# Performance work log

Hardware: AMD Instinct MI355X
Metric: run time of the kernel (lower is better)

Reference implementation:

```python
import jax, jax.numpy as jnp
import numpy as np

B, C, H, W = 4, 256, 64, 64
CQK = C // 8


def setup_inputs() -> dict:
    key = jax.random.key(0)
    ks = jax.random.split(key, 7)
    s = 1.0 / np.sqrt(C)
    return {
        "x": jax.random.normal(ks[0], (B, C, H, W), dtype=jnp.float32),
        "Wq": jax.random.normal(ks[1], (CQK, C), dtype=jnp.float32) * s,
        "bq": jax.random.normal(ks[2], (CQK,), dtype=jnp.float32) * 0.01,
        "Wk": jax.random.normal(ks[3], (CQK, C), dtype=jnp.float32) * s,
        "bk": jax.random.normal(ks[4], (CQK,), dtype=jnp.float32) * 0.01,
        "Wv": jax.random.normal(ks[5], (C, C), dtype=jnp.float32) * s,
        "bv": jax.random.normal(ks[6], (C,), dtype=jnp.float32) * 0.01,
    }


def reference(x, Wq, bq, Wk, bk, Wv, bv):
    b, c, h, w = x.shape
    n = h * w
    xf = x.reshape(b, c, n)                                   # [B,C,N]
    # 1x1 convs == per-pixel channel projections
    q = jnp.einsum('oc,bcn->bon', Wq, xf) + bq[None, :, None]  # [B,C/8,N]
    k = jnp.einsum('oc,bcn->bon', Wk, xf) + bk[None, :, None]  # [B,C/8,N]
    v = jnp.einsum('oc,bcn->bon', Wv, xf) + bv[None, :, None]  # [B,C,N]
    # energy[b,i,j] = <q[:, i], k[:, j]>  (no scaling, as in the original)
    energy = jnp.einsum('boi,boj->bij', q, k)                  # [B,N,N]
    attn = jax.nn.softmax(energy, axis=-1)                     # [B,N,N]
    # out[b,c,i] = sum_j v[b,c,j] * attn[b,i,j]
    out = jnp.einsum('bcj,bij->bci', v, attn)                  # [B,C,N]
    return out.reshape(b, c, h, w) + x
```

## Files before the change

### kernel.cpp

```cpp
#include <hip/hip_runtime.h>
#include <hip/hip_bf16.h>
#include <math.h>

#define B_DIM 4
#define C_DIM 256
#define CQK_DIM 32
#define N_POS 4096
#define NPART 4

typedef unsigned short u16;
typedef __attribute__((ext_vector_type(8))) short bf16x8;
typedef __attribute__((ext_vector_type(4))) float f32x4;

__device__ __forceinline__ u16 f32_to_bf16_rn(float f) {
    union { float f; unsigned int u; } v; v.f = f;
    unsigned int u = v.u;
    u += 0x7fffu + ((u >> 16) & 1u);
    return (u16)(u >> 16);
}
__device__ __forceinline__ float bf16_to_f32(u16 h) {
    union { unsigned int u; float f; } v; v.u = ((unsigned int)h) << 16;
    return v.f;
}
__device__ __forceinline__ unsigned pk_bf16(float a, float b) {
    unsigned r;
    asm("v_cvt_pk_bf16_f32 %0, %1, %2" : "=v"(r) : "v"(a), "v"(b));
    return r;
}
__device__ __forceinline__ void async_copy16(const u16* g, u16* l) {
    __builtin_amdgcn_global_load_lds(
        (const __attribute__((address_space(1))) void*)g,
        (__attribute__((address_space(3))) void*)l, 16, 0, 0);
}


__global__ __launch_bounds__(256) void proj_kernel(
    const float* __restrict__ x,
    const float* __restrict__ Wq, const float* __restrict__ bq,
    const float* __restrict__ Wk, const float* __restrict__ bk,
    const float* __restrict__ Wv, const float* __restrict__ bv,
    u16* __restrict__ qhi, u16* __restrict__ qlo,
    u16* __restrict__ kth, u16* __restrict__ ktl,
    u16* __restrict__ vtile)
{
    const int t    = threadIdx.x;
    const int blk  = blockIdx.x;
    const int b    = blk >> 6;
    const int jt   = blk & 63;
    const int n0   = jt * 64;
    const int wave = t >> 6;
    const int lane = t & 63;
    const int n16  = lane & 15;
    const int quad = lane >> 4;
    const float* xb = x + (size_t)b * C_DIM * N_POS;

    f32x4 accV[4][4];
    f32x4 accQ[4];
    #pragma unroll
    for (int v = 0; v < 4; ++v)
        #pragma unroll
        for (int nt = 0; nt < 4; ++nt) accV[v][nt] = (f32x4){0.f,0.f,0.f,0.f};
    #pragma unroll
    for (int nt = 0; nt < 4; ++nt) accQ[nt] = (f32x4){0.f,0.f,0.f,0.f};

    const float* Wqk  = (wave < 2) ? Wq : Wk;
    const int    qkrow = (wave & 1) * 16 + n16;

    for (int kk = 0; kk < 8; ++kk) {
        const int k0 = kk * 32 + quad * 8;
        bf16x8 bh[4], bl[4];
        #pragma unroll
        for (int nt = 0; nt < 4; ++nt) {
            const float* xp = xb + (size_t)k0 * N_POS + n0 + nt * 16 + n16;
            float xv[8];
            #pragma unroll
            for (int j = 0; j < 8; ++j) xv[j] = xp[(size_t)j * N_POS];
            #pragma unroll
            for (int j = 0; j < 8; ++j) {
                u16 h = f32_to_bf16_rn(xv[j]);
                bh[nt][j] = (short)h;
                bl[nt][j] = (short)f32_to_bf16_rn(xv[j] - bf16_to_f32(h));
            }
        }
        #pragma unroll
        for (int v = 0; v < 4; ++v) {
            const float* wr = Wv + (size_t)(wave * 64 + v * 16 + n16) * C_DIM + k0;
            float4 a0 = *(const float4*)(wr);
            float4 a1 = *(const float4*)(wr + 4);
            bf16x8 ah;
            ah[0] = (short)f32_to_bf16_rn(a0.x); ah[1] = (short)f32_to_bf16_rn(a0.y);
            ah[2] = (short)f32_to_bf16_rn(a0.z); ah[3] = (short)f32_to_bf16_rn(a0.w);
            ah[4] = (short)f32_to_bf16_rn(a1.x); ah[5] = (short)f32_to_bf16_rn(a1.y);
            ah[6] = (short)f32_to_bf16_rn(a1.z); ah[7] = (short)f32_to_bf16_rn(a1.w);
            #pragma unroll
            for (int nt = 0; nt < 4; ++nt)
                accV[v][nt] = __builtin_amdgcn_mfma_f32_16x16x32_bf16(
                    ah, bh[nt], accV[v][nt], 0, 0, 0);
        }
        {
            const float* wr = Wqk + (size_t)qkrow * C_DIM + k0;
            bf16x8 ah, al;
            #pragma unroll
            for (int j = 0; j < 8; ++j) {
                float w = wr[j];
                u16 h = f32_to_bf16_rn(w);
                ah[j] = (short)h;
                al[j] = (short)f32_to_bf16_rn(w - bf16_to_f32(h));
            }
            #pragma unroll
            for (int nt = 0; nt < 4; ++nt) {
                accQ[nt] = __builtin_amdgcn_mfma_f32_16x16x32_bf16(ah, bh[nt], accQ[nt], 0, 0, 0);
                accQ[nt] = __builtin_amdgcn_mfma_f32_16x16x32_bf16(ah, bl[nt], accQ[nt], 0, 0, 0);
                accQ[nt] = __builtin_amdgcn_mfma_f32_16x16x32_bf16(al, bh[nt], accQ[nt], 0, 0, 0);
            }
        }
    }

    u16* vt = vtile + (size_t)(b * 64 + jt) * (32 * 512);
    #pragma unroll
    for (int v = 0; v < 4; ++v) {
        const int cb = wave * 4 + v;
        #pragma unroll
        for (int r = 0; r < 4; ++r) {
            const int c = cb * 16 + quad * 4 + r;
            const float bias = bv[c];
            #pragma unroll
            for (int nt = 0; nt < 4; ++nt) {
                const int kb = nt >> 1;
                vt[(cb * 2 + kb) * 512
                   + ((n16 >> 2) * 16 + quad * 4 + r) * 8
                   + (nt & 1) * 4 + (n16 & 3)] =
                    f32_to_bf16_rn(accV[v][nt][r] + bias);
            }
        }
    }
    if (wave < 2) {
        #pragma unroll
        for (int r = 0; r < 4; ++r) {
            const int c = (wave & 1) * 16 + quad * 4 + r;
            const float bias = bq[c];
            #pragma unroll
            for (int nt = 0; nt < 4; ++nt) {
                float val = accQ[nt][r] + bias;
                u16 h = f32_to_bf16_rn(val);
                u16 lo = f32_to_bf16_rn(val - bf16_to_f32(h));
                size_t base = ((size_t)b * N_POS + n0 + nt * 16 + n16) * CQK_DIM + c;
                qhi[base] = h; qlo[base] = lo;
            }
        }
    } else {
        u16* kh_t = kth + (size_t)(b * 64 + jt) * (4 * 512);
        u16* kl_t = ktl + (size_t)(b * 64 + jt) * (4 * 512);
        #pragma unroll
        for (int r = 0; r < 4; ++r) {
            const int c = (wave & 1) * 16 + quad * 4 + r;
            const float bias = bk[c];
            #pragma unroll
            for (int nt = 0; nt < 4; ++nt) {
                float val = accQ[nt][r] + bias;
                u16 h = f32_to_bf16_rn(val);
                u16 lo = f32_to_bf16_rn(val - bf16_to_f32(h));
                const int off = nt * 512 + ((c >> 3) * 16 + n16) * 8 + (c & 7);
                kh_t[off] = h; kl_t[off] = lo;
            }
        }
    }
}

__global__ __launch_bounds__(256, 2) void flash_kernel(
    const u16* __restrict__ qhi, const u16* __restrict__ qlo,
    const u16* __restrict__ kth, const u16* __restrict__ ktl,
    const u16* __restrict__ vtile,
    u16* __restrict__ part, float2* __restrict__ ml)
{
    __shared__ u16 Vt[2][40 * 512];

    const int t    = threadIdx.x;
    const int wave = t >> 6;
    const int lane = t & 63;
    const int n16  = lane & 15;
    const int quad = lane >> 4;

    const int idx    = blockIdx.x;
    const int xcd    = idx & 7;
    const int b      = xcd & 3;
    const int z      = idx >> 3;
    const int p      = z & 3;
    const int iouter = z >> 2;
    const int itile  = (iouter << 1) | (xcd >> 2);
    const int i0     = itile * 128 + wave * 32;

    bf16x8 qh[2], ql[2];
    #pragma unroll
    for (int m = 0; m < 2; ++m) {
        qh[m] = *(const bf16x8*)(qhi + ((size_t)b * N_POS + i0 + m * 16 + n16) * CQK_DIM + quad * 8);
        ql[m] = *(const bf16x8*)(qlo + ((size_t)b * N_POS + i0 + m * 16 + n16) * CQK_DIM + quad * 8);
    }

    f32x4 O[2][16];
    #pragma unroll
    for (int m = 0; m < 2; ++m)
        #pragma unroll
        for (int cb = 0; cb < 16; ++cb) O[m][cb] = (f32x4){0.f, 0.f, 0.f, 0.f};
    float lsum[2] = {0.f, 0.f};

    const int jt_beg = p * 16;
    const int jt_end = jt_beg + 16;

    const u16* vb_base = vtile + (size_t)b * 64 * (32 * 512);
    const u16* kh_base = kth   + (size_t)b * 64 * (4 * 512);
    const u16* kl_base = ktl   + (size_t)b * 64 * (4 * 512);

#define STAGE(JT, BUF)                                                          \
    {                                                                           \
        const u16* vsrc  = vb_base + (size_t)(JT) * (32 * 512);                 \
        const u16* khsrc = kh_base + (size_t)(JT) * (4 * 512);                  \
        const u16* klsrc = kl_base + (size_t)(JT) * (4 * 512);                  \
        for (int ch = wave; ch < 32; ch += 4)                                   \
            async_copy16(vsrc + ch * 512 + lane * 8, Vt[BUF] + ch * 512);       \
        for (int ch = wave; ch < 8; ch += 4)                                    \
            async_copy16((ch < 4 ? khsrc + ch * 512 : klsrc + (ch - 4) * 512)   \
                             + lane * 8,                                        \
                         Vt[BUF] + (32 + ch) * 512);                            \
    }

    STAGE(jt_beg, 0);

    int buf = 0;
    for (int jt = jt_beg; jt < jt_end; ++jt) {
        __syncthreads();

        if (jt + 1 < jt_end) STAGE(jt + 1, buf ^ 1);

        const u16* kbuf = Vt[buf];
        bf16x8 kh[4], kl[4];
        #pragma unroll
        for (int jb = 0; jb < 4; ++jb) {
            kh[jb] = *(const bf16x8*)(kbuf + (32 + jb) * 512 + lane * 8);
            kl[jb] = *(const bf16x8*)(kbuf + (36 + jb) * 512 + lane * 8);
        }

        f32x4 s[2][4];
        __builtin_amdgcn_s_setprio(1);
        #pragma unroll
        for (int m = 0; m < 2; ++m)
            #pragma unroll
            for (int jb = 0; jb < 4; ++jb) {
                f32x4 acc = (f32x4){0.f, 0.f, 0.f, 0.f};
                acc = __builtin_amdgcn_mfma_f32_16x16x32_bf16(kh[jb], qh[m], acc, 0, 0, 0);
                acc = __builtin_amdgcn_mfma_f32_16x16x32_bf16(kl[jb], qh[m], acc, 0, 0, 0);
                acc = __builtin_amdgcn_mfma_f32_16x16x32_bf16(kh[jb], ql[m], acc, 0, 0, 0);
                s[m][jb] = acc;
            }
        __builtin_amdgcn_s_setprio(0);

        bf16x8 Pf[2][2];
        #pragma unroll
        for (int m = 0; m < 2; ++m)
            #pragma unroll
            for (int kb = 0; kb < 2; ++kb) {
                union { bf16x8 v; unsigned u[4]; } tmp;
                #pragma unroll
                for (int j2 = 0; j2 < 2; ++j2) {
                    const int jb = kb * 2 + j2;
                    float p0 = __expf(s[m][jb][0]);
                    float p1 = __expf(s[m][jb][1]);
                    float p2 = __expf(s[m][jb][2]);
                    float p3 = __expf(s[m][jb][3]);
                    lsum[m] += (p0 + p1) + (p2 + p3);
                    tmp.u[j2 * 2 + 0] = pk_bf16(p0, p1);
                    tmp.u[j2 * 2 + 1] = pk_bf16(p2, p3);
                }
                Pf[m][kb] = tmp.v;
            }

        const u16* vb = Vt[buf];
        __builtin_amdgcn_s_setprio(1);
        #pragma unroll
        for (int kb = 0; kb < 2; ++kb) {
            #pragma unroll
            for (int cb = 0; cb < 16; ++cb) {
                bf16x8 Vf = *(const bf16x8*)(vb + (cb * 2 + kb) * 512 + lane * 8);
                #pragma unroll
                for (int m = 0; m < 2; ++m)
                    O[m][cb] = __builtin_amdgcn_mfma_f32_16x16x32_bf16(
                        Pf[m][kb], Vf, O[m][cb], 0, 0, 0);
            }
        }
        __builtin_amdgcn_s_setprio(0);
        buf ^= 1;
    }
#undef STAGE

    #pragma unroll
    for (int m = 0; m < 2; ++m) {
        lsum[m] += __shfl_xor(lsum[m], 16, 64);
        lsum[m] += __shfl_xor(lsum[m], 32, 64);
    }
    float inv_l[2][4];
    #pragma unroll
    for (int m = 0; m < 2; ++m)
        #pragma unroll
        for (int r = 0; r < 4; ++r)
            inv_l[m][r] = 1.f / __shfl(lsum[m], quad * 4 + r, 64);

    u16* pbase = part + ((size_t)(p * 4 + b) * N_POS + i0) * C_DIM;
    #pragma unroll
    for (int m = 0; m < 2; ++m)
        #pragma unroll
        for (int cb = 0; cb < 16; ++cb)
            #pragma unroll
            for (int r = 0; r < 4; ++r)
                pbase[(size_t)(m * 16 + quad * 4 + r) * C_DIM + cb * 16 + n16] =
                    f32_to_bf16_rn(O[m][cb][r] * inv_l[m][r]);
    if (quad == 0) {
        #pragma unroll
        for (int m = 0; m < 2; ++m)
            ml[(size_t)(p * 4 + b) * N_POS + i0 + m * 16 + n16] =
                make_float2(0.f, lsum[m]);
    }
}

__global__ __launch_bounds__(256) void reduce_kernel(
    const u16* __restrict__ part, const float2* __restrict__ ml,
    const float* __restrict__ x, float* __restrict__ out)
{
    const int TJ = 32;
    __shared__ float wgt[NPART][TJ];
    __shared__ float trans[C_DIM][TJ + 1];

    const int t   = threadIdx.x;
    const int blk = blockIdx.x;
    const int b   = blk >> 7;
    const int n0  = (blk & 127) * TJ;

    if (t < TJ) {
        int i = n0 + t;
        float s = 0.f, w[NPART];
        #pragma unroll
        for (int p = 0; p < NPART; ++p) {
            float2 a = ml[(size_t)(p * 4 + b) * N_POS + i];
            w[p] = a.y;
            s += w[p];
        }
        float inv = 1.f / s;
        #pragma unroll
        for (int p = 0; p < NPART; ++p) wgt[p][t] = w[p] * inv;
    }
    __syncthreads();

    {
        const int cp = t & 127;
        const int ih = t >> 7;
        for (int ib = 0; ib < TJ; ib += 2) {
            int i = ib + ih;
            float acc0 = 0.f, acc1 = 0.f;
            #pragma unroll
            for (int p = 0; p < NPART; ++p) {
                const u16* row = part + ((size_t)(p * 4 + b) * N_POS + n0 + i) * C_DIM;
                ushort2 pv = ((const ushort2*)row)[cp];
                float wp = wgt[p][i];
                acc0 += wp * bf16_to_f32(pv.x);
                acc1 += wp * bf16_to_f32(pv.y);
            }
            trans[2 * cp][i]     = acc0;
            trans[2 * cp + 1][i] = acc1;
        }
    }
    __syncthreads();

    {
        const int il = t & 31;
        const int cr = t >> 5;
        const float* xb = x + (size_t)b * C_DIM * N_POS;
        float* ob       = out + (size_t)b * C_DIM * N_POS;
        for (int cc = 0; cc < 32; ++cc) {
            int c = cc * 8 + cr;
            size_t g = (size_t)c * N_POS + n0 + il;
            ob[g] = trans[c][il] + xb[g];
        }
    }
}

extern "C" void kernel_launch(void* const* d_in, const int* in_sizes, int n_in,
                              void* d_out, int out_size, void* d_ws, size_t ws_size,
                              hipStream_t stream) {
    const float* x  = (const float*)d_in[0];
    const float* Wq = (const float*)d_in[1];
    const float* bq = (const float*)d_in[2];
    const float* Wk = (const float*)d_in[3];
    const float* bk = (const float*)d_in[4];
    const float* Wv = (const float*)d_in[5];
    const float* bv = (const float*)d_in[6];
    float* out = (float*)d_out;

    char* ws = (char*)d_ws;
    u16*    qhi   = (u16*)(ws);
    u16*    qlo   = (u16*)(ws + (1ull << 20));
    u16*    kth   = (u16*)(ws + (2ull << 20));
    u16*    ktl   = (u16*)(ws + (3ull << 20));
    u16*    vtile = (u16*)(ws + (4ull << 20));
    u16*    part  = (u16*)(ws + (12ull << 20));
    float2* mlp   = (float2*)(ws + (44ull << 20));

    hipLaunchKernelGGL(proj_kernel, dim3(256), dim3(256), 0, stream,
                       x, Wq, bq, Wk, bk, Wv, bv, qhi, qlo, kth, ktl, vtile);
    hipLaunchKernelGGL(flash_kernel, dim3(512), dim3(256), 0, stream,
                       qhi, qlo, kth, ktl, vtile, part, mlp);
    hipLaunchKernelGGL(reduce_kernel, dim3(512), dim3(256), 0, stream,
                       part, mlp, x, out);
}
```

Baseline: 88.51 us.

## Pre-convert weights to bf16, halve proj tiles, use exp2 softmax, vectorize reduce

Adds a small kernel that converts Wv, Wq and Wk to bf16 (with hi/lo splits for Q/K) once per call, so the projection kernel no longer repeats the conversion in every block. The projection kernel now processes 32 positions per block across 512 blocks to improve occupancy. Q is pre-scaled by log2(e) so the flash kernel can use exp2f instead of __expf. The reduce kernel reads 8 bf16 values per load instead of 2. The trade-offs are an extra kernel launch and reuse of the part workspace region for the converted weights, which is only safe because the flash kernel writes part after the projection kernel has finished.

```diff
diff --git a/kernel.cpp b/kernel.cpp
--- a/kernel.cpp
+++ b/kernel.cpp
@@ -7,6 +7,7 @@
 #define CQK_DIM 32
 #define N_POS 4096
 #define NPART 4
+#define LOG2E 1.4426950408889634f
 
 typedef unsigned short u16;
 typedef __attribute__((ext_vector_type(8))) short bf16x8;
@@ -34,43 +35,68 @@
 }
 
 
+__global__ __launch_bounds__(256) void wconv_kernel(
+    const float* __restrict__ Wv, const float* __restrict__ Wq,
+    const float* __restrict__ Wk,
+    u16* __restrict__ Wvh, u16* __restrict__ Wqh, u16* __restrict__ Wql,
+    u16* __restrict__ Wkh, u16* __restrict__ Wkl)
+{
+    const int i = blockIdx.x * 256 + threadIdx.x;
+    const int stride = gridDim.x * 256;
+    for (int k = i; k < C_DIM * C_DIM; k += stride)
+        Wvh[k] = f32_to_bf16_rn(Wv[k]);
+    for (int k = i; k < CQK_DIM * C_DIM; k += stride) {
+        float w = Wq[k];
+        u16 h = f32_to_bf16_rn(w);
+        Wqh[k] = h; Wql[k] = f32_to_bf16_rn(w - bf16_to_f32(h));
+        w = Wk[k];
+        h = f32_to_bf16_rn(w);
+        Wkh[k] = h; Wkl[k] = f32_to_bf16_rn(w - bf16_to_f32(h));
+    }
+}
+
 __global__ __launch_bounds__(256) void proj_kernel(
     const float* __restrict__ x,
-    const float* __restrict__ Wq, const float* __restrict__ bq,
-    const float* __restrict__ Wk, const float* __restrict__ bk,
-    const float* __restrict__ Wv, const float* __restrict__ bv,
+    const u16* __restrict__ Wvh, const u16* __restrict__ Wqh,
+    const u16* __restrict__ Wql, const u16* __restrict__ Wkh,
+    const u16* __restrict__ Wkl,
+    const float* __restrict__ bq, const float* __restrict__ bk,
+    const float* __restrict__ bv,
     u16* __restrict__ qhi, u16* __restrict__ qlo,
     u16* __restrict__ kth, u16* __restrict__ ktl,
     u16* __restrict__ vtile)
 {
     const int t    = threadIdx.x;
     const int blk  = blockIdx.x;
-    const int b    = blk >> 6;
-    const int jt   = blk & 63;
-    const int n0   = jt * 64;
+    const int b    = blk >> 7;
+    const int jt32 = blk & 127;
+    const int n0   = jt32 * 32;
+    const int jt64 = jt32 >> 1;
+    const int half = jt32 & 1;
     const int wave = t >> 6;
     const int lane = t & 63;
     const int n16  = lane & 15;
     const int quad = lane >> 4;
     const float* xb = x + (size_t)b * C_DIM * N_POS;
 
-    f32x4 accV[4][4];
-    f32x4 accQ[4];
+    f32x4 accV[4][2];
+    f32x4 accQ[2];
     #pragma unroll
     for (int v = 0; v < 4; ++v)
         #pragma unroll
-        for (int nt = 0; nt < 4; ++nt) accV[v][nt] = (f32x4){0.f,0.f,0.f,0.f};
-    #pragma unroll
-    for (int nt = 0; nt < 4; ++nt) accQ[nt] = (f32x4){0.f,0.f,0.f,0.f};
-
-    const float* Wqk  = (wave < 2) ? Wq : Wk;
-    const int    qkrow = (wave & 1) * 16 + n16;
+        for (int nt = 0; nt < 2; ++nt) accV[v][nt] = (f32x4){0.f,0.f,0.f,0.f};
+    #pragma unroll
+    for (int nt = 0; nt < 2; ++nt) accQ[nt] = (f32x4){0.f,0.f,0.f,0.f};
+
+    const u16* Wqk_h = (wave < 2) ? Wqh : Wkh;
+    const u16* Wqk_l = (wave < 2) ? Wql : Wkl;
+    const int  qkrow = (wave & 1) * 16 + n16;
 
     for (int kk = 0; kk < 8; ++kk) {
         const int k0 = kk * 32 + quad * 8;
-        bf16x8 bh[4], bl[4];
-        #pragma unroll
-        for (int nt = 0; nt < 4; ++nt) {
+        bf16x8 bh[2], bl[2];
+        #pragma unroll
+        for (int nt = 0; nt < 2; ++nt) {
             const float* xp = xb + (size_t)k0 * N_POS + n0 + nt * 16 + n16;
             float xv[8];
             #pragma unroll
@@ -84,31 +110,17 @@
         }
         #pragma unroll
         for (int v = 0; v < 4; ++v) {
-            const float* wr = Wv + (size_t)(wave * 64 + v * 16 + n16) * C_DIM + k0;
-            float4 a0 = *(const float4*)(wr);
-            float4 a1 = *(const float4*)(wr + 4);
-            bf16x8 ah;
-            ah[0] = (short)f32_to_bf16_rn(a0.x); ah[1] = (short)f32_to_bf16_rn(a0.y);
-            ah[2] = (short)f32_to_bf16_rn(a0.z); ah[3] = (short)f32_to_bf16_rn(a0.w);
-            ah[4] = (short)f32_to_bf16_rn(a1.x); ah[5] = (short)f32_to_bf16_rn(a1.y);
-            ah[6] = (short)f32_to_bf16_rn(a1.z); ah[7] = (short)f32_to_bf16_rn(a1.w);
-            #pragma unroll
-            for (int nt = 0; nt < 4; ++nt)
+            bf16x8 ah = *(const bf16x8*)(Wvh + (size_t)(wave * 64 + v * 16 + n16) * C_DIM + k0);
+            #pragma unroll
+            for (int nt = 0; nt < 2; ++nt)
                 accV[v][nt] = __builtin_amdgcn_mfma_f32_16x16x32_bf16(
                     ah, bh[nt], accV[v][nt], 0, 0, 0);
         }
         {
-            const float* wr = Wqk + (size_t)qkrow * C_DIM + k0;
-            bf16x8 ah, al;
-            #pragma unroll
-            for (int j = 0; j < 8; ++j) {
-                float w = wr[j];
-                u16 h = f32_to_bf16_rn(w);
-                ah[j] = (short)h;
-                al[j] = (short)f32_to_bf16_rn(w - bf16_to_f32(h));
-            }
-            #pragma unroll
-            for (int nt = 0; nt < 4; ++nt) {
+            bf16x8 ah = *(const bf16x8*)(Wqk_h + (size_t)qkrow * C_DIM + k0);
+            bf16x8 al = *(const bf16x8*)(Wqk_l + (size_t)qkrow * C_DIM + k0);
+            #pragma unroll
+            for (int nt = 0; nt < 2; ++nt) {
                 accQ[nt] = __builtin_amdgcn_mfma_f32_16x16x32_bf16(ah, bh[nt], accQ[nt], 0, 0, 0);
                 accQ[nt] = __builtin_amdgcn_mfma_f32_16x16x32_bf16(ah, bl[nt], accQ[nt], 0, 0, 0);
                 accQ[nt] = __builtin_amdgcn_mfma_f32_16x16x32_bf16(al, bh[nt], accQ[nt], 0, 0, 0);
@@ -116,7 +128,7 @@
         }
     }
 
-    u16* vt = vtile + (size_t)(b * 64 + jt) * (32 * 512);
+    u16* vt = vtile + (size_t)(b * 64 + jt64) * (32 * 512);
     #pragma unroll
     for (int v = 0; v < 4; ++v) {
         const int cb = wave * 4 + v;
@@ -125,11 +137,10 @@
             const int c = cb * 16 + quad * 4 + r;
             const float bias = bv[c];
             #pragma unroll
-            for (int nt = 0; nt < 4; ++nt) {
-                const int kb = nt >> 1;
-                vt[(cb * 2 + kb) * 512
+            for (int nt = 0; nt < 2; ++nt) {
+                vt[(cb * 2 + half) * 512
                    + ((n16 >> 2) * 16 + quad * 4 + r) * 8
-                   + (nt & 1) * 4 + (n16 & 3)] =
+                   + nt * 4 + (n16 & 3)] =
                     f32_to_bf16_rn(accV[v][nt][r] + bias);
             }
         }
@@ -140,8 +151,8 @@
             const int c = (wave & 1) * 16 + quad * 4 + r;
             const float bias = bq[c];
             #pragma unroll
-            for (int nt = 0; nt < 4; ++nt) {
-                float val = accQ[nt][r] + bias;
+            for (int nt = 0; nt < 2; ++nt) {
+                float val = (accQ[nt][r] + bias) * LOG2E;
                 u16 h = f32_to_bf16_rn(val);
                 u16 lo = f32_to_bf16_rn(val - bf16_to_f32(h));
                 size_t base = ((size_t)b * N_POS + n0 + nt * 16 + n16) * CQK_DIM + c;
@@ -149,18 +160,19 @@
             }
         }
     } else {
-        u16* kh_t = kth + (size_t)(b * 64 + jt) * (4 * 512);
-        u16* kl_t = ktl + (size_t)(b * 64 + jt) * (4 * 512);
+        u16* kh_t = kth + (size_t)(b * 64 + jt64) * (4 * 512);
+        u16* kl_t = ktl + (size_t)(b * 64 + jt64) * (4 * 512);
         #pragma unroll
         for (int r = 0; r < 4; ++r) {
             const int c = (wave & 1) * 16 + quad * 4 + r;
             const float bias = bk[c];
             #pragma unroll
-            for (int nt = 0; nt < 4; ++nt) {
+            for (int nt = 0; nt < 2; ++nt) {
                 float val = accQ[nt][r] + bias;
                 u16 h = f32_to_bf16_rn(val);
                 u16 lo = f32_to_bf16_rn(val - bf16_to_f32(h));
-                const int off = nt * 512 + ((c >> 3) * 16 + n16) * 8 + (c & 7);
+                const int jb = half * 2 + nt;
+                const int off = jb * 512 + ((c >> 3) * 16 + n16) * 8 + (c & 7);
                 kh_t[off] = h; kl_t[off] = lo;
             }
         }
@@ -263,10 +275,10 @@
                 #pragma unroll
                 for (int j2 = 0; j2 < 2; ++j2) {
                     const int jb = kb * 2 + j2;
-                    float p0 = __expf(s[m][jb][0]);
-                    float p1 = __expf(s[m][jb][1]);
-                    float p2 = __expf(s[m][jb][2]);
-                    float p3 = __expf(s[m][jb][3]);
+                    float p0 = exp2f(s[m][jb][0]);
+                    float p1 = exp2f(s[m][jb][1]);
+                    float p2 = exp2f(s[m][jb][2]);
+                    float p3 = exp2f(s[m][jb][3]);
                     lsum[m] += (p0 + p1) + (p2 + p3);
                     tmp.u[j2 * 2 + 0] = pk_bf16(p0, p1);
                     tmp.u[j2 * 2 + 1] = pk_bf16(p2, p3);
@@ -350,21 +362,23 @@
     __syncthreads();
 
     {
-        const int cp = t & 127;
-        const int ih = t >> 7;
-        for (int ib = 0; ib < TJ; ib += 2) {
-            int i = ib + ih;
-            float acc0 = 0.f, acc1 = 0.f;
+        const int cp = t & 31;
+        const int ih = t >> 5;
+        for (int ib = 0; ib < TJ; ib += 8) {
+            const int i = ib + ih;
+            float acc[8] = {0.f, 0.f, 0.f, 0.f, 0.f, 0.f, 0.f, 0.f};
             #pragma unroll
             for (int p = 0; p < NPART; ++p) {
                 const u16* row = part + ((size_t)(p * 4 + b) * N_POS + n0 + i) * C_DIM;
-                ushort2 pv = ((const ushort2*)row)[cp];
-                float wp = wgt[p][i];
-                acc0 += wp * bf16_to_f32(pv.x);
-                acc1 += wp * bf16_to_f32(pv.y);
-            }
-            trans[2 * cp][i]     = acc0;
-            trans[2 * cp + 1][i] = acc1;
+                bf16x8 pv = *(const bf16x8*)(row + cp * 8);
+                const float wp = wgt[p][i];
+                #pragma unroll
+                for (int e = 0; e < 8; ++e)
+                    acc[e] += wp * bf16_to_f32((u16)pv[e]);
+            }
+            #pragma unroll
+            for (int e = 0; e < 8; ++e)
+                trans[cp * 8 + e][i] = acc[e];
         }
     }
     __syncthreads();
@@ -403,8 +417,17 @@
     u16*    part  = (u16*)(ws + (12ull << 20));
     float2* mlp   = (float2*)(ws + (44ull << 20));
 
-    hipLaunchKernelGGL(proj_kernel, dim3(256), dim3(256), 0, stream,
-                       x, Wq, bq, Wk, bk, Wv, bv, qhi, qlo, kth, ktl, vtile);
+    u16* Wvh = (u16*)(ws + (12ull << 20));
+    u16* Wqh = (u16*)(ws + (12ull << 20) + 131072);
+    u16* Wql = (u16*)(ws + (12ull << 20) + 131072 + 16384);
+    u16* Wkh = (u16*)(ws + (12ull << 20) + 131072 + 32768);
+    u16* Wkl = (u16*)(ws + (12ull << 20) + 131072 + 49152);
+
+    hipLaunchKernelGGL(wconv_kernel, dim3(64), dim3(256), 0, stream,
+                       Wv, Wq, Wk, Wvh, Wqh, Wql, Wkh, Wkl);
+    hipLaunchKernelGGL(proj_kernel, dim3(512), dim3(256), 0, stream,
+                       x, Wvh, Wqh, Wql, Wkh, Wkl, bq, bk, bv,
+                       qhi, qlo, kth, ktl, vtile);
     hipLaunchKernelGGL(flash_kernel, dim3(512), dim3(256), 0, stream,
                        qhi, qlo, kth, ktl, vtile, part, mlp);
     hipLaunchKernelGGL(reduce_kernel, dim3(512), dim3(256), 0, stream,
```

After: 99.20 us. 1.12x slower.
